# Performance work log

Measured on AMD Instinct MI355X. Metric: run time of the kernel, lower is better.

The kernel has to match this reference:

```python
import jax, jax.numpy as jnp
import numpy as np

B, H, W, C = 2, 64, 64, 256
NH, K = 8, 7  # num_heads, neighborhood kernel size


def setup_inputs() -> dict:
    key = jax.random.key(0)
    ks = jax.random.split(key, 8)
    xav = lambda k, shape: jax.random.normal(k, shape, jnp.float32) * np.sqrt(2.0 / (shape[0] + shape[1])).astype(np.float32)
    return {
        "x": jax.random.normal(ks[0], (B, H, W, C), jnp.float32),
        "norm1_g": jnp.ones((C,), jnp.float32),
        "norm1_b": jnp.zeros((C,), jnp.float32),
        "qkv_w": xav(ks[1], (3 * C, C)),
        "qkv_b": jnp.zeros((3 * C,), jnp.float32),
        "rpb": jax.random.normal(ks[2], (NH, 2 * K - 1, 2 * K - 1), jnp.float32) * 0.02,
        "proj_w": xav(ks[3], (C, C)),
        "proj_b": jnp.zeros((C,), jnp.float32),
        "norm2_g": jnp.ones((C,), jnp.float32),
        "norm2_b": jnp.zeros((C,), jnp.float32),
        "fc1_w": xav(ks[4], (4 * C, C)),
        "fc1_b": jnp.zeros((4 * C,), jnp.float32),
        "fc2_w": xav(ks[5], (C, 4 * C)),
        "fc2_b": jnp.zeros((C,), jnp.float32),
    }


def _layernorm(x, g, b, eps=1e-5):
    m = x.mean(-1, keepdims=True)
    v = jnp.mean((x - m) ** 2, axis=-1, keepdims=True)
    return (x - m) * jax.lax.rsqrt(v + eps) * g + b


def _nat2d(x, qkv_w, qkv_b, rpb, proj_w, proj_b):
    """Neighborhood attention 2D (NATTEN semantics: edge-clamped k x k windows,
    relative positional bias indexed by key_pos - query_pos + k - 1)."""
    b, h, w, c = x.shape
    nh = rpb.shape[0]
    k = (rpb.shape[1] + 1) // 2
    dh = c // nh
    qkv = (x @ qkv_w.T + qkv_b).reshape(b, h, w, 3, nh, dh)
    q = qkv[..., 0, :, :] * (dh ** -0.5)  # [b,h,w,nh,dh]
    kk = qkv[..., 1, :, :]
    vv = qkv[..., 2, :, :]
    # edge-clamped window starts per query row/col
    starts_h = jnp.clip(jnp.arange(h) - k // 2, 0, h - k)
    starts_w = jnp.clip(jnp.arange(w) - k // 2, 0, w - k)
    idx_h = starts_h[:, None] + jnp.arange(k)  # [h,k] key row indices
    idx_w = starts_w[:, None] + jnp.arange(k)  # [w,k] key col indices
    # gather neighborhoods -> [b,h,w,k,k,nh,dh]
    knb = kk[:, idx_h][:, :, :, idx_w].transpose(0, 1, 3, 2, 4, 5, 6)
    vnb = vv[:, idx_h][:, :, :, idx_w].transpose(0, 1, 3, 2, 4, 5, 6)
    attn = jnp.einsum('bijhd,bijklhd->bijhkl', q, knb)  # [b,h,w,nh,k,k]
    # relative positional bias: index = key - query + (k-1) in [0, 2k-2]
    rb_h = idx_h - jnp.arange(h)[:, None] + (k - 1)  # [h,k]
    rb_w = idx_w - jnp.arange(w)[:, None] + (k - 1)  # [w,k]
    bias = rpb[:, rb_h][:, :, :, rb_w]  # [nh,h,k,w,k]
    bias = bias.transpose(1, 3, 0, 2, 4)  # [h,w,nh,k,k]
    attn = jax.nn.softmax((attn + bias).reshape(b, h, w, nh, k * k), axis=-1)
    out = jnp.einsum('bijhn,bijnhd->bijhd', attn, vnb.reshape(b, h, w, k * k, nh, dh))
    return out.reshape(b, h, w, c) @ proj_w.T + proj_b


def reference(x, norm1_g, norm1_b, qkv_w, qkv_b, rpb, proj_w, proj_b,
              norm2_g, norm2_b, fc1_w, fc1_b, fc2_w, fc2_b):
    # norm -> neighborhood attention -> residual
    x = x + _nat2d(_layernorm(x, norm1_g, norm1_b), qkv_w, qkv_b, rpb, proj_w, proj_b)
    # norm -> MLP (gelu) -> residual
    hdn = _layernorm(x, norm2_g, norm2_b)
    hdn = jax.nn.gelu(hdn @ fc1_w.T + fc1_b, approximate=False)
    return x + (hdn @ fc2_w.T + fc2_b)
```

## Files before the change

kernel.cpp:

```cpp
#include <hip/hip_runtime.h>

typedef __attribute__((ext_vector_type(8))) short bf16x8;
typedef __attribute__((ext_vector_type(4))) float f32x4;
typedef unsigned short u16;

__device__ __forceinline__ float bf2f(u16 u) {
    return __builtin_bit_cast(float, ((unsigned int)u) << 16);
}
__device__ __forceinline__ u16 f2bf(float f) {
    unsigned int x = __builtin_bit_cast(unsigned int, f);
    x += 0x7FFFu + ((x >> 16) & 1u);
    return (u16)(x >> 16);
}

typedef const __attribute__((address_space(1))) void* gas_t;
typedef __attribute__((address_space(3))) void* las_t;
__device__ __forceinline__ void load_lds16(const u16* g, u16* l) {
    __builtin_amdgcn_global_load_lds((gas_t)g, (las_t)l, 16, 0, 0);
}

__global__ __launch_bounds__(256) void cvt_kernel(
    const float* __restrict__ s0, const float* __restrict__ s1,
    const float* __restrict__ s2, const float* __restrict__ s3,
    u16* __restrict__ dst)
{
    const int i4 = (blockIdx.x * 256 + threadIdx.x) * 4;
    const float* src;
    int off;
    if      (i4 < 196608) { src = s0; off = i4; }
    else if (i4 < 262144) { src = s1; off = i4 - 196608; }
    else if (i4 < 524288) { src = s2; off = i4 - 262144; }
    else                  { src = s3; off = i4 - 524288; }
    float4 v = *(const float4*)(src + off);
    ushort4 o;
    o.x = f2bf(v.x); o.y = f2bf(v.y); o.z = f2bf(v.z); o.w = f2bf(v.w);
    *(ushort4*)(dst + i4) = o;
}

__global__ __launch_bounds__(256) void ln_kernel(
    const float* __restrict__ x, const float* __restrict__ g,
    const float* __restrict__ b, u16* __restrict__ y)
{
    const int tok  = blockIdx.x * 4 + (threadIdx.x >> 6);
    const int lane = threadIdx.x & 63;
    float4 v = *(const float4*)(x + (size_t)tok * 256 + lane * 4);
    float s  = v.x + v.y + v.z + v.w;
    float sq = v.x*v.x + v.y*v.y + v.z*v.z + v.w*v.w;
    #pragma unroll
    for (int off = 32; off; off >>= 1) {
        s  += __shfl_xor(s, off);
        sq += __shfl_xor(sq, off);
    }
    float mean = s * (1.0f / 256.0f);
    float var  = sq * (1.0f / 256.0f) - mean * mean;
    float rs   = rsqrtf(var + 1e-5f);
    float4 gv = *(const float4*)(g + lane * 4);
    float4 bv = *(const float4*)(b + lane * 4);
    ushort4 o;
    o.x = f2bf((v.x - mean) * rs * gv.x + bv.x);
    o.y = f2bf((v.y - mean) * rs * gv.y + bv.y);
    o.z = f2bf((v.z - mean) * rs * gv.z + bv.z);
    o.w = f2bf((v.w - mean) * rs * gv.w + bv.w);
    *(ushort4*)(y + (size_t)tok * 256 + lane * 4) = o;
}

template<int N, int K, int EPI>
__global__ __launch_bounds__(256) void gemm64(
    const u16* __restrict__ A, const u16* __restrict__ W,
    const float* __restrict__ bias, const float* __restrict__ res,
    void* __restrict__ outv)
{
    __shared__ u16 As[64 * 64];
    __shared__ u16 Bs[64 * 64];
    const int tid  = threadIdx.x;
    const int lane = tid & 63;
    const int wave = tid >> 6;
    const int m0   = blockIdx.x * 64;
    const int n0   = blockIdx.y * 64;
    const int wm0  = (wave >> 1) * 32;
    const int wn0  = (wave & 1) * 32;

    f32x4 acc[2][2];
    #pragma unroll
    for (int mt = 0; mt < 2; ++mt)
        #pragma unroll
        for (int nt = 0; nt < 2; ++nt)
            acc[mt][nt] = (f32x4){0.f, 0.f, 0.f, 0.f};

    int soff[2];
    #pragma unroll
    for (int r = 0; r < 2; ++r) {
        const int s   = r * 256 + tid;
        const int row = s >> 3;
        const int c   = (s & 7) ^ (row & 7);
        soff[r] = row * K + c * 8;
    }
    const int fr = lane & 15;
    const int fc = lane >> 4;

    for (int k0 = 0; k0 < K; k0 += 64) {
        __syncthreads();
        #pragma unroll
        for (int r = 0; r < 2; ++r) {
            load_lds16(A + (size_t)m0 * K + k0 + soff[r], As + (r * 256 + tid) * 8);
            load_lds16(W + (size_t)n0 * K + k0 + soff[r], Bs + (r * 256 + tid) * 8);
        }
        __syncthreads();
        #pragma unroll
        for (int ks = 0; ks < 2; ++ks) {
            bf16x8 af[2], bw[2];
            #pragma unroll
            for (int mt = 0; mt < 2; ++mt) {
                const int rr   = wm0 + mt * 16 + fr;
                const int phys = (ks * 4 + fc) ^ (rr & 7);
                af[mt] = *(const bf16x8*)(As + rr * 64 + phys * 8);
            }
            #pragma unroll
            for (int nt = 0; nt < 2; ++nt) {
                const int rr   = wn0 + nt * 16 + fr;
                const int phys = (ks * 4 + fc) ^ (rr & 7);
                bw[nt] = *(const bf16x8*)(Bs + rr * 64 + phys * 8);
            }
            #pragma unroll
            for (int mt = 0; mt < 2; ++mt)
                #pragma unroll
                for (int nt = 0; nt < 2; ++nt)
                    acc[mt][nt] = __builtin_amdgcn_mfma_f32_16x16x32_bf16(af[mt], bw[nt], acc[mt][nt], 0, 0, 0);
        }
    }

    const int col = lane & 15;
    const int rb  = (lane >> 4) * 4;
    #pragma unroll
    for (int nt = 0; nt < 2; ++nt) {
        const int n  = n0 + wn0 + nt * 16 + col;
        const float bv = bias[n];
        #pragma unroll
        for (int mt = 0; mt < 2; ++mt) {
            #pragma unroll
            for (int r = 0; r < 4; ++r) {
                const int m = m0 + wm0 + mt * 16 + rb + r;
                float v = acc[mt][nt][r] + bv;
                if (EPI == 1) {
                    if (n < 256) v *= 0.1767766952966369f;
                    ((u16*)outv)[(size_t)m * N + n] = f2bf(v);
                }
                if (EPI == 2) {
                    v += res[(size_t)m * N + n];
                    ((float*)outv)[(size_t)m * N + n] = v;
                }
                if (EPI == 3) {
                    v = 0.5f * v * (1.0f + erff(v * 0.7071067811865475f));
                    ((u16*)outv)[(size_t)m * N + n] = f2bf(v);
                }
            }
        }
    }
}

__global__ __launch_bounds__(256, 2) void attn_tile_kernel(
    const u16* __restrict__ qkv, const float* __restrict__ rpb,
    u16* __restrict__ out)
{
    __shared__ u16   kv[100 * 64];
    __shared__ u16   qs[16 * 32];
    __shared__ float probs[16 * 66];

    const int tid  = threadIdx.x;
    const int bb   = blockIdx.x >> 8;
    const int rem  = blockIdx.x & 255;
    const int ti0  = (rem >> 4) << 2;
    const int tj0  = (rem & 15) << 2;
    const int oh   = min(max(ti0 - 3, 0), 54);
    const int ow   = min(max(tj0 - 3, 0), 54);
    const int tokbase = bb * 4096;

    int off_kv[4];
    #pragma unroll
    for (int r = 0; r < 4; ++r) {
        const int s  = r * 256 + tid;
        const int t  = s >> 3;
        const int cs = s & 7;
        const int c  = cs ^ (t & 7);
        const int tr = t / 10, tc = t - tr * 10;
        const int tokg = tokbase + (oh + tr) * 64 + (ow + tc);
        off_kv[r] = tokg * 768 + 256 + ((c & 4) << 6) + (c & 3) * 8;
    }
    const int tq   = tid >> 2;
    const int qoff = (tokbase + (ti0 + (tq >> 2)) * 64 + (tj0 + (tq & 3))) * 768
                   + (tid & 3) * 8;

    const int token = tid >> 4;
    const int part  = tid & 15;
    const int li = token >> 2, lj = token & 3;
    const int i  = ti0 + li,   j  = tj0 + lj;
    const int sh = min(max(i - 3, 0), 57);
    const int sw = min(max(j - 3, 0), 57);
    const int rowbase  = (sh - oh) * 10 + (sw - ow);
    const int rb_const = (sh - i + 6) * 13 + (sw - j + 6);
    const size_t outbase = (size_t)(tokbase + i * 64 + j) * 256 + part * 2;

    for (int h = 0; h < 8; ++h) {
        __syncthreads();
        const int hoff = h * 32;
        #pragma unroll
        for (int r = 0; r < 3; ++r)
            load_lds16(qkv + off_kv[r] + hoff, kv + (r * 256 + tid) * 8);
        if (tid < 32)
            load_lds16(qkv + off_kv[3] + hoff, kv + (768 + tid) * 8);
        if (tid < 64)
            load_lds16(qkv + qoff + hoff, qs + tid * 8);
        __syncthreads();

        float qv[32];
        #pragma unroll
        for (int c = 0; c < 4; ++c) {
            bf16x8 v = *(const bf16x8*)(qs + token * 32 + c * 8);
            #pragma unroll
            for (int e = 0; e < 8; ++e) qv[c * 8 + e] = bf2f((u16)v[e]);
        }

        float sc[4];
        #pragma unroll
        for (int sidx = 0; sidx < 4; ++sidx) {
            const int n = part + sidx * 16;
            if (n < 49) {
                const int kh = n / 7, kw = n - (n / 7) * 7;
                const int hidx = rowbase + kh * 10 + kw;
                float acc = rpb[h * 169 + rb_const + kh * 13 + kw];
                #pragma unroll
                for (int c = 0; c < 4; ++c) {
                    const int slot = (hidx << 3) + (c ^ (hidx & 7));
                    bf16x8 kk = *(const bf16x8*)(kv + slot * 8);
                    #pragma unroll
                    for (int e = 0; e < 8; ++e)
                        acc += qv[c * 8 + e] * bf2f((u16)kk[e]);
                }
                sc[sidx] = acc;
            } else {
                sc[sidx] = -1e30f;
            }
        }
        float mx = fmaxf(fmaxf(sc[0], sc[1]), fmaxf(sc[2], sc[3]));
        #pragma unroll
        for (int off = 1; off < 16; off <<= 1) mx = fmaxf(mx, __shfl_xor(mx, off));
        float ex[4], ssum = 0.f;
        #pragma unroll
        for (int sidx = 0; sidx < 4; ++sidx) {
            ex[sidx] = __expf(sc[sidx] - mx);
            ssum += ex[sidx];
        }
        #pragma unroll
        for (int off = 1; off < 16; off <<= 1) ssum += __shfl_xor(ssum, off);
        const float inv = 1.0f / ssum;
        #pragma unroll
        for (int sidx = 0; sidx < 4; ++sidx)
            probs[token * 66 + part + sidx * 16] = ex[sidx] * inv;
        __syncthreads();

        float o0 = 0.f, o1 = 0.f;
        const int vchunk = 4 + (part >> 2);
        const int vsub   = (part & 3) * 2;
        #pragma unroll
        for (int kh = 0; kh < 7; ++kh) {
            #pragma unroll
            for (int kw = 0; kw < 7; ++kw) {
                const int n    = kh * 7 + kw;
                const int hidx = rowbase + kh * 10 + kw;
                const float p  = probs[token * 66 + n];
                const int slot = (hidx << 3) + (vchunk ^ (hidx & 7));
                const unsigned int vv = *(const unsigned int*)(kv + slot * 8 + vsub);
                o0 += p * bf2f((u16)(vv & 0xffffu));
                o1 += p * bf2f((u16)(vv >> 16));
            }
        }
        ushort2 ov;
        ov.x = f2bf(o0); ov.y = f2bf(o1);
        *(ushort2*)(out + outbase + hoff) = ov;
    }
}

extern "C" void kernel_launch(void* const* d_in, const int* in_sizes, int n_in,
                              void* d_out, int out_size, void* d_ws, size_t ws_size,
                              hipStream_t stream)
{
    const float* x      = (const float*)d_in[0];
    const float* n1g    = (const float*)d_in[1];
    const float* n1b    = (const float*)d_in[2];
    const float* qkv_w  = (const float*)d_in[3];
    const float* qkv_b  = (const float*)d_in[4];
    const float* rpb    = (const float*)d_in[5];
    const float* proj_w = (const float*)d_in[6];
    const float* proj_b = (const float*)d_in[7];
    const float* n2g    = (const float*)d_in[8];
    const float* n2b    = (const float*)d_in[9];
    const float* fc1_w  = (const float*)d_in[10];
    const float* fc1_b  = (const float*)d_in[11];
    const float* fc2_w  = (const float*)d_in[12];
    const float* fc2_b  = (const float*)d_in[13];
    float* out = (float*)d_out;

    char* wsb = (char*)d_ws;
    u16*   wbf   = (u16*)wsb;
    u16*   qkvW  = wbf;
    u16*   projW = wbf + 196608;
    u16*   fc1W  = wbf + 262144;
    u16*   fc2W  = wbf + 524288;
    u16*   ln1   = (u16*)(wsb + 1572864);
    u16*   attn  = ln1;
    u16*   qkvB  = (u16*)(wsb + 5767168);
    u16*   ln2   = qkvB;
    u16*   hbuf  = (u16*)(wsb + 9961472);
    float* x1    = (float*)(wsb + 26738688);

    dim3 blk(256);
    cvt_kernel<<<768, blk, 0, stream>>>(qkv_w, proj_w, fc1_w, fc2_w, wbf);
    ln_kernel<<<2048, blk, 0, stream>>>(x, n1g, n1b, ln1);
    gemm64<768, 256, 1><<<dim3(128, 12), blk, 0, stream>>>(ln1, qkvW, qkv_b, nullptr, qkvB);
    attn_tile_kernel<<<512, blk, 0, stream>>>(qkvB, rpb, attn);
    gemm64<256, 256, 2><<<dim3(128, 4), blk, 0, stream>>>(attn, projW, proj_b, x, x1);
    ln_kernel<<<2048, blk, 0, stream>>>(x1, n2g, n2b, ln2);
    gemm64<1024, 256, 3><<<dim3(128, 16), blk, 0, stream>>>(ln2, fc1W, fc1_b, nullptr, hbuf);
    gemm64<256, 1024, 2><<<dim3(128, 4), blk, 0, stream>>>(hbuf, fc2W, fc2_b, x1, out);
}
```

Baseline: 165.1 us.

## Fuse weight conversion with LN1, fuse proj GEMM with LN2, enlarge GEMM tiles

Merges the weight fp32-to-bf16 conversion into the first layernorm kernel and fuses the projection GEMM, residual add and second layernorm into one kernel that holds full 256-wide rows. The generic GEMM now uses 128-row tiles (128 or 64 columns) with a K step of 32 and a new LDS swizzle. Together this cuts two launches and removes an intermediate round trip through global memory. In exchange the k-loop syncs twice as often, the larger tiles launch fewer blocks, and the proj+LN kernel runs only 128 blocks.

```diff
diff --git a/kernel.cpp b/kernel.cpp
--- a/kernel.cpp
+++ b/kernel.cpp
@@ -12,6 +12,7 @@
     x += 0x7FFFu + ((x >> 16) & 1u);
     return (u16)(x >> 16);
 }
+__device__ __forceinline__ int swz(int row) { return (row ^ (row >> 2)) & 3; }
 
 typedef const __attribute__((address_space(1))) void* gas_t;
 typedef __attribute__((address_space(3))) void* las_t;
@@ -19,30 +20,31 @@
     __builtin_amdgcn_global_load_lds((gas_t)g, (las_t)l, 16, 0, 0);
 }
 
-__global__ __launch_bounds__(256) void cvt_kernel(
+__global__ __launch_bounds__(256) void prep_kernel(
+    const float* __restrict__ x, const float* __restrict__ g, const float* __restrict__ b,
     const float* __restrict__ s0, const float* __restrict__ s1,
     const float* __restrict__ s2, const float* __restrict__ s3,
-    u16* __restrict__ dst)
+    u16* __restrict__ wbf, u16* __restrict__ y)
 {
-    const int i4 = (blockIdx.x * 256 + threadIdx.x) * 4;
-    const float* src;
-    int off;
-    if      (i4 < 196608) { src = s0; off = i4; }
-    else if (i4 < 262144) { src = s1; off = i4 - 196608; }
-    else if (i4 < 524288) { src = s2; off = i4 - 262144; }
-    else                  { src = s3; off = i4 - 524288; }
-    float4 v = *(const float4*)(src + off);
-    ushort4 o;
-    o.x = f2bf(v.x); o.y = f2bf(v.y); o.z = f2bf(v.z); o.w = f2bf(v.w);
-    *(ushort4*)(dst + i4) = o;
-}
-
-__global__ __launch_bounds__(256) void ln_kernel(
-    const float* __restrict__ x, const float* __restrict__ g,
-    const float* __restrict__ b, u16* __restrict__ y)
-{
-    const int tok  = blockIdx.x * 4 + (threadIdx.x >> 6);
-    const int lane = threadIdx.x & 63;
+    const int bid = blockIdx.x, tid = threadIdx.x;
+    {
+        int idx = bid * 256 + tid;
+        #pragma unroll
+        for (int r = 0; r < 2; ++r) {
+            if (r == 1) {
+                if (tid >= 128) break;
+                idx = 524288 + bid * 128 + tid;
+            }
+            const float* src; int off;
+            if      (idx < 196608) { src = s0; off = idx; }
+            else if (idx < 262144) { src = s1; off = idx - 196608; }
+            else if (idx < 524288) { src = s2; off = idx - 262144; }
+            else                   { src = s3; off = idx - 524288; }
+            wbf[idx] = f2bf(src[off]);
+        }
+    }
+    const int tok  = bid * 4 + (tid >> 6);
+    const int lane = tid & 63;
     float4 v = *(const float4*)(x + (size_t)tok * 256 + lane * 4);
     float s  = v.x + v.y + v.z + v.w;
     float sq = v.x*v.x + v.y*v.y + v.z*v.z + v.w*v.w;
@@ -51,9 +53,9 @@
         s  += __shfl_xor(s, off);
         sq += __shfl_xor(sq, off);
     }
-    float mean = s * (1.0f / 256.0f);
-    float var  = sq * (1.0f / 256.0f) - mean * mean;
-    float rs   = rsqrtf(var + 1e-5f);
+    const float mean = s * (1.0f / 256.0f);
+    const float var  = sq * (1.0f / 256.0f) - mean * mean;
+    const float rs   = rsqrtf(var + 1e-5f);
     float4 gv = *(const float4*)(g + lane * 4);
     float4 bv = *(const float4*)(b + lane * 4);
     ushort4 o;
@@ -64,79 +66,82 @@
     *(ushort4*)(y + (size_t)tok * 256 + lane * 4) = o;
 }
 
-template<int N, int K, int EPI>
-__global__ __launch_bounds__(256) void gemm64(
+template<int BN, int N, int K, int EPI>
+__global__ __launch_bounds__(256) void gemm_m97(
     const u16* __restrict__ A, const u16* __restrict__ W,
     const float* __restrict__ bias, const float* __restrict__ res,
     void* __restrict__ outv)
 {
-    __shared__ u16 As[64 * 64];
-    __shared__ u16 Bs[64 * 64];
+    constexpr int MT = (BN == 128) ? 4 : 2;
+    constexpr int NT = 4;
+    __shared__ u16 As[128 * 32];
+    __shared__ u16 Bs[BN * 32];
     const int tid  = threadIdx.x;
     const int lane = tid & 63;
     const int wave = tid >> 6;
-    const int m0   = blockIdx.x * 64;
-    const int n0   = blockIdx.y * 64;
-    const int wm0  = (wave >> 1) * 32;
-    const int wn0  = (wave & 1) * 32;
-
-    f32x4 acc[2][2];
-    #pragma unroll
-    for (int mt = 0; mt < 2; ++mt)
-        #pragma unroll
-        for (int nt = 0; nt < 2; ++nt)
+    const int m0   = blockIdx.x * 128;
+    const int n0   = blockIdx.y * BN;
+    const int wm0  = (BN == 128) ? (wave >> 1) * 64 : wave * 32;
+    const int wn0  = (BN == 128) ? (wave & 1) * 64 : 0;
+
+    f32x4 acc[MT][NT];
+    #pragma unroll
+    for (int mt = 0; mt < MT; ++mt)
+        #pragma unroll
+        for (int nt = 0; nt < NT; ++nt)
             acc[mt][nt] = (f32x4){0.f, 0.f, 0.f, 0.f};
 
-    int soff[2];
+    int aoff[2], boff[BN / 64];
     #pragma unroll
     for (int r = 0; r < 2; ++r) {
         const int s   = r * 256 + tid;
-        const int row = s >> 3;
-        const int c   = (s & 7) ^ (row & 7);
-        soff[r] = row * K + c * 8;
+        const int row = s >> 2;
+        aoff[r] = row * K + ((s & 3) ^ swz(row)) * 8;
+    }
+    #pragma unroll
+    for (int r = 0; r < BN / 64; ++r) {
+        const int s   = r * 256 + tid;
+        const int row = s >> 2;
+        boff[r] = row * K + ((s & 3) ^ swz(row)) * 8;
     }
     const int fr = lane & 15;
-    const int fc = lane >> 4;
-
-    for (int k0 = 0; k0 < K; k0 += 64) {
-        __syncthreads();
-        #pragma unroll
-        for (int r = 0; r < 2; ++r) {
-            load_lds16(A + (size_t)m0 * K + k0 + soff[r], As + (r * 256 + tid) * 8);
-            load_lds16(W + (size_t)n0 * K + k0 + soff[r], Bs + (r * 256 + tid) * 8);
-        }
-        __syncthreads();
-        #pragma unroll
-        for (int ks = 0; ks < 2; ++ks) {
-            bf16x8 af[2], bw[2];
+    const int lc = lane >> 4;
+
+    for (int k0 = 0; k0 < K; k0 += 32) {
+        __syncthreads();
+        #pragma unroll
+        for (int r = 0; r < 2; ++r)
+            load_lds16(A + (size_t)m0 * K + k0 + aoff[r], As + (r * 256 + tid) * 8);
+        #pragma unroll
+        for (int r = 0; r < BN / 64; ++r)
+            load_lds16(W + (size_t)n0 * K + k0 + boff[r], Bs + (r * 256 + tid) * 8);
+        __syncthreads();
+        bf16x8 af[MT], bw[NT];
+        #pragma unroll
+        for (int mt = 0; mt < MT; ++mt) {
+            const int rr = wm0 + mt * 16 + fr;
+            af[mt] = *(const bf16x8*)(As + rr * 32 + (lc ^ swz(rr)) * 8);
+        }
+        #pragma unroll
+        for (int nt = 0; nt < NT; ++nt) {
+            const int rr = wn0 + nt * 16 + fr;
+            bw[nt] = *(const bf16x8*)(Bs + rr * 32 + (lc ^ swz(rr)) * 8);
+        }
+        #pragma unroll
+        for (int mt = 0; mt < MT; ++mt)
             #pragma unroll
-            for (int mt = 0; mt < 2; ++mt) {
-                const int rr   = wm0 + mt * 16 + fr;
-                const int phys = (ks * 4 + fc) ^ (rr & 7);
-                af[mt] = *(const bf16x8*)(As + rr * 64 + phys * 8);
-            }
-            #pragma unroll
-            for (int nt = 0; nt < 2; ++nt) {
-                const int rr   = wn0 + nt * 16 + fr;
-                const int phys = (ks * 4 + fc) ^ (rr & 7);
-                bw[nt] = *(const bf16x8*)(Bs + rr * 64 + phys * 8);
-            }
-            #pragma unroll
-            for (int mt = 0; mt < 2; ++mt)
-                #pragma unroll
-                for (int nt = 0; nt < 2; ++nt)
-                    acc[mt][nt] = __builtin_amdgcn_mfma_f32_16x16x32_bf16(af[mt], bw[nt], acc[mt][nt], 0, 0, 0);
-        }
+            for (int nt = 0; nt < NT; ++nt)
+                acc[mt][nt] = __builtin_amdgcn_mfma_f32_16x16x32_bf16(af[mt], bw[nt], acc[mt][nt], 0, 0, 0);
     }
 
     const int col = lane & 15;
     const int rb  = (lane >> 4) * 4;
     #pragma unroll
-    for (int nt = 0; nt < 2; ++nt) {
+    for (int nt = 0; nt < NT; ++nt) {
         const int n  = n0 + wn0 + nt * 16 + col;
         const float bv = bias[n];
         #pragma unroll
-        for (int mt = 0; mt < 2; ++mt) {
+        for (int mt = 0; mt < MT; ++mt) {
             #pragma unroll
             for (int r = 0; r < 4; ++r) {
                 const int m = m0 + wm0 + mt * 16 + rb + r;
@@ -158,6 +163,95 @@
     }
 }
 
+__global__ __launch_bounds__(256) void proj_ln_kernel(
+    const u16* __restrict__ A, const u16* __restrict__ W, const float* __restrict__ pb,
+    const float* __restrict__ xres, const float* __restrict__ g2, const float* __restrict__ b2,
+    float* __restrict__ x1, u16* __restrict__ ln2out)
+{
+    __shared__ u16 As[64 * 32];
+    __shared__ u16 Bs[256 * 32];
+    const int tid  = threadIdx.x;
+    const int lane = tid & 63;
+    const int wave = tid >> 6;
+    const int m0   = blockIdx.x * 64;
+
+    f32x4 acc[16];
+    #pragma unroll
+    for (int nt = 0; nt < 16; ++nt) acc[nt] = (f32x4){0.f, 0.f, 0.f, 0.f};
+
+    const int arow = tid >> 2, acs = tid & 3;
+    const int aoff = (m0 + arow) * 256 + (acs ^ (arow & 3)) * 8;
+    int boff[4];
+    #pragma unroll
+    for (int r = 0; r < 4; ++r) {
+        const int s   = r * 256 + tid;
+        const int row = s >> 2;
+        boff[r] = row * 256 + ((s & 3) ^ (row & 3)) * 8;
+    }
+    const int fr = lane & 15;
+    const int fc = lane >> 4;
+
+    for (int k0 = 0; k0 < 256; k0 += 32) {
+        __syncthreads();
+        load_lds16(A + aoff + k0, As + tid * 8);
+        #pragma unroll
+        for (int r = 0; r < 4; ++r)
+            load_lds16(W + boff[r] + k0, Bs + (r * 256 + tid) * 8);
+        __syncthreads();
+        const int ra = wave * 16 + fr;
+        bf16x8 af = *(const bf16x8*)(As + ra * 32 + (fc ^ (ra & 3)) * 8);
+        #pragma unroll
+        for (int nt = 0; nt < 16; ++nt) {
+            const int rbq = nt * 16 + fr;
+            bf16x8 bw = *(const bf16x8*)(Bs + rbq * 32 + (fc ^ (rbq & 3)) * 8);
+            acc[nt] = __builtin_amdgcn_mfma_f32_16x16x32_bf16(af, bw, acc[nt], 0, 0, 0);
+        }
+    }
+
+    const int col = lane & 15;
+    const int g   = lane >> 4;
+    float s[4] = {0.f, 0.f, 0.f, 0.f}, sq[4] = {0.f, 0.f, 0.f, 0.f};
+    #pragma unroll
+    for (int nt = 0; nt < 16; ++nt) {
+        const int n = nt * 16 + col;
+        const float bv = pb[n];
+        #pragma unroll
+        for (int r = 0; r < 4; ++r) {
+            const int m = m0 + wave * 16 + g * 4 + r;
+            float v = acc[nt][r] + bv + xres[(size_t)m * 256 + n];
+            acc[nt][r] = v;
+            s[r] += v; sq[r] += v * v;
+        }
+    }
+    #pragma unroll
+    for (int off = 1; off < 16; off <<= 1) {
+        #pragma unroll
+        for (int r = 0; r < 4; ++r) {
+            s[r]  += __shfl_xor(s[r], off);
+            sq[r] += __shfl_xor(sq[r], off);
+        }
+    }
+    float mean[4], rs[4];
+    #pragma unroll
+    for (int r = 0; r < 4; ++r) {
+        mean[r] = s[r] * (1.0f / 256.0f);
+        const float var = sq[r] * (1.0f / 256.0f) - mean[r] * mean[r];
+        rs[r] = rsqrtf(var + 1e-5f);
+    }
+    #pragma unroll
+    for (int nt = 0; nt < 16; ++nt) {
+        const int n = nt * 16 + col;
+        const float gam = g2[n], bet = b2[n];
+        #pragma unroll
+        for (int r = 0; r < 4; ++r) {
+            const int m = m0 + wave * 16 + g * 4 + r;
+            const float v = acc[nt][r];
+            x1[(size_t)m * 256 + n] = v;
+            ln2out[(size_t)m * 256 + n] = f2bf((v - mean[r]) * rs[r] * gam + bet);
+        }
+    }
+}
+
 __global__ __launch_bounds__(256, 2) void attn_tile_kernel(
     const u16* __restrict__ qkv, const float* __restrict__ rpb,
     u16* __restrict__ out)
@@ -180,8 +274,7 @@
     for (int r = 0; r < 4; ++r) {
         const int s  = r * 256 + tid;
         const int t  = s >> 3;
-        const int cs = s & 7;
-        const int c  = cs ^ (t & 7);
+        const int c  = (s & 7) ^ (t & 7);
         const int tr = t / 10, tc = t - tr * 10;
         const int tokg = tokbase + (oh + tr) * 64 + (ow + tc);
         off_kv[r] = tokg * 768 + 256 + ((c & 4) << 6) + (c & 3) * 8;
@@ -307,19 +400,17 @@
     u16*   fc1W  = wbf + 262144;
     u16*   fc2W  = wbf + 524288;
     u16*   ln1   = (u16*)(wsb + 1572864);
-    u16*   attn  = ln1;
+    u16*   attnB = ln1;
     u16*   qkvB  = (u16*)(wsb + 5767168);
     u16*   ln2   = qkvB;
     u16*   hbuf  = (u16*)(wsb + 9961472);
     float* x1    = (float*)(wsb + 26738688);
 
     dim3 blk(256);
-    cvt_kernel<<<768, blk, 0, stream>>>(qkv_w, proj_w, fc1_w, fc2_w, wbf);
-    ln_kernel<<<2048, blk, 0, stream>>>(x, n1g, n1b, ln1);
-    gemm64<768, 256, 1><<<dim3(128, 12), blk, 0, stream>>>(ln1, qkvW, qkv_b, nullptr, qkvB);
-    attn_tile_kernel<<<512, blk, 0, stream>>>(qkvB, rpb, attn);
-    gemm64<256, 256, 2><<<dim3(128, 4), blk, 0, stream>>>(attn, projW, proj_b, x, x1);
-    ln_kernel<<<2048, blk, 0, stream>>>(x1, n2g, n2b, ln2);
-    gemm64<1024, 256, 3><<<dim3(128, 16), blk, 0, stream>>>(ln2, fc1W, fc1_b, nullptr, hbuf);
-    gemm64<256, 1024, 2><<<dim3(128, 4), blk, 0, stream>>>(hbuf, fc2W, fc2_b, x1, out);
-}
+    prep_kernel<<<2048, blk, 0, stream>>>(x, n1g, n1b, qkv_w, proj_w, fc1_w, fc2_w, wbf, ln1);
+    gemm_m97<128, 768, 256, 1><<<dim3(64, 6), blk, 0, stream>>>(ln1, qkvW, qkv_b, nullptr, qkvB);
+    attn_tile_kernel<<<512, blk, 0, stream>>>(qkvB, rpb, attnB);
+    proj_ln_kernel<<<128, blk, 0, stream>>>(attnB, projW, proj_b, x, n2g, n2b, x1, ln2);
+    gemm_m97<128, 1024, 256, 3><<<dim3(64, 8), blk, 0, stream>>>(ln2, fc1W, fc1_b, nullptr, hbuf);
+    gemm_m97<64, 256, 1024, 2><<<dim3(64, 4), blk, 0, stream>>>(hbuf, fc2W, fc2_b, x1, out);
+}
```

New measurement: 173.9 us. 5.3% more time.
